# Performance work log

Measured on AMD Instinct MI355X. Metric: run time of the kernel, lower is better.

## Reference

```python
import jax, jax.numpy as jnp
import numpy as np

H = 2048      # hidden_size
F = 768       # moe_intermediate_size
E = 32        # num_experts
K = 4         # num_experts_per_tok (top_k)
SF = 5632     # shared_expert_intermediate_size
B, S = 1, 2048


def setup_inputs() -> dict:
    key = jax.random.key(0)
    ks = jax.random.split(key, 9)
    rn = lambda k, sh, sc: (jax.random.normal(k, sh, jnp.float32) * sc)
    return {
        "hidden_states": rn(ks[0], (B, S, H), 1.0),
        "gate_w": rn(ks[1], (H, E), 0.02),                 # router Linear(H->E), no bias
        "wg": rn(ks[2], (E, H, F), H ** -0.5),             # expert gate_proj
        "wu": rn(ks[3], (E, H, F), H ** -0.5),             # expert up_proj
        "wd": rn(ks[4], (E, F, H), F ** -0.5),             # expert down_proj
        "sg": rn(ks[5], (H, SF), H ** -0.5),               # shared expert gate_proj
        "su": rn(ks[6], (H, SF), H ** -0.5),               # shared expert up_proj
        "sd": rn(ks[7], (SF, H), SF ** -0.5),              # shared expert down_proj
        "seg": rn(ks[8], (H, 1), H ** -0.5),               # shared_expert_gate Linear(H->1)
    }


def _moe_forward(x, gate_w, wg, wu, wd, sg, su, sd, seg):
    # x: [T, H] flattened tokens
    T = x.shape[0]
    logits = x @ gate_w                                    # [T, E]
    probs = jax.nn.softmax(logits, axis=-1)
    topw, topi = jax.lax.top_k(probs, K)                   # [T, K]
    topw = topw / jnp.sum(topw, axis=-1, keepdims=True)    # norm_topk_prob=True
    # dense combine weights [T, E] (expert ids per token are unique -> set is safe)
    combine = jnp.zeros((T, E), x.dtype).at[jnp.arange(T)[:, None], topi].set(topw)

    def body(acc, ew):
        wg_e, wu_e, wd_e, c_e = ew                         # [H,F],[H,F],[F,H],[T]
        h = jax.nn.silu(x @ wg_e) * (x @ wu_e)             # [T, F]
        return acc + c_e[:, None] * (h @ wd_e), None

    out, _ = jax.lax.scan(body, jnp.zeros_like(x), (wg, wu, wd, combine.T))

    shared = (jax.nn.silu(x @ sg) * (x @ su)) @ sd         # [T, H]
    out = out + jax.nn.sigmoid(x @ seg) * shared
    return out


def reference(hidden_states, gate_w, wg, wu, wd, sg, su, sd, seg):
    b, s, h = hidden_states.shape
    x = hidden_states.reshape(-1, h)
    out = _moe_forward(x, gate_w, wg, wu, wd, sg, su, sd, seg)
    return out.reshape(b, s, h)
```

## Files before the change

kernel.cpp:

```cpp
#include <hip/hip_runtime.h>
#include <hip/hip_bf16.h>
#include <math.h>

#define H_DIM 2048
#define F_DIM 768
#define E_NUM 32
#define TOPK 4
#define SF_DIM 5632
#define T_NUM 2048
#define P_MAX (T_NUM * TOPK)
#define KSPLIT 4

#define NB_GU_SHARED ((SF_DIM / 64) * (T_NUM / 128))
#define NB_GU_EXPERT ((F_DIM / 64) * (T_NUM / 128) * E_NUM)
#define NB_DN_SHARED ((H_DIM / 128) * (T_NUM / 128) * KSPLIT)
#define NB_DN_EXPERT ((H_DIM / 128) * (T_NUM / 128) * E_NUM)

typedef __attribute__((ext_vector_type(8))) short short8v;
typedef __attribute__((ext_vector_type(4))) float f4;
typedef unsigned short u16;

__device__ __forceinline__ u16 f2b(float f) {
  unsigned int u = __float_as_uint(f);
  u += 0x7FFFu + ((u >> 16) & 1u);
  return (u16)(u >> 16);
}

__device__ __forceinline__ f4 mfma16(short8v a, short8v b, f4 c) {
  return __builtin_amdgcn_mfma_f32_16x16x32_bf16(a, b, c, 0, 0, 0);
}

__device__ __forceinline__ void gld16(const u16* g, u16* l) {
  __builtin_amdgcn_global_load_lds(
      (const __attribute__((address_space(1))) void*)g,
      (__attribute__((address_space(3))) void*)l, 16, 0, 0);
}

__global__ __launch_bounds__(64) void router_kernel(
    const float* __restrict__ x, const float* __restrict__ gate_w,
    const float* __restrict__ seg, int* __restrict__ cnt,
    int* __restrict__ toklist, int* __restrict__ slotE,
    int* __restrict__ slotPos, float* __restrict__ wt4,
    float* __restrict__ sigbuf) {
  const int t = blockIdx.x;
  const int l = threadIdx.x;
  const int e = l & 31;
  const int half = l >> 5;
  const float* xr = x + (size_t)t * H_DIM;

  float acc = 0.0f, aseg = 0.0f;
  const int h0 = half * (H_DIM / 2);
  for (int h = 0; h < H_DIM / 2; ++h) {
    float xv = xr[h0 + h];
    acc += xv * gate_w[(h0 + h) * E_NUM + e];
    aseg += xv * seg[h0 + h];
  }
  acc += __shfl_xor(acc, 32, 64);
  aseg += __shfl_xor(aseg, 32, 64);

  float m = acc;
#pragma unroll
  for (int mask = 16; mask >= 1; mask >>= 1) m = fmaxf(m, __shfl_xor(m, mask, 64));
  float p = expf(acc - m);
  float s = p;
#pragma unroll
  for (int mask = 16; mask >= 1; mask >>= 1) s += __shfl_xor(s, mask, 64);
  p /= s;

  float pv = p;
  int ids[TOPK];
  float wv[TOPK];
  float wsum = 0.0f;
#pragma unroll
  for (int k = 0; k < TOPK; ++k) {
    float mv = pv;
    int mi = e;
#pragma unroll
    for (int mask = 16; mask >= 1; mask >>= 1) {
      float ov = __shfl_xor(mv, mask, 64);
      int oi = __shfl_xor(mi, mask, 64);
      if (ov > mv || (ov == mv && oi < mi)) { mv = ov; mi = oi; }
    }
    ids[k] = mi;
    wv[k] = mv;
    wsum += mv;
    if (e == mi) pv = -1.0f;
  }

  if (l < TOPK) {
    int id = ids[l];
    float w = wv[l] / wsum;
    int pos = atomicAdd(&cnt[id], 1);
    toklist[id * T_NUM + pos] = t;
    slotE[t * TOPK + l] = id;
    slotPos[t * TOPK + l] = pos;
    wt4[t * TOPK + l] = w;
  }
  if (l == 0) sigbuf[t] = 1.0f / (1.0f + expf(-aseg));
}

__global__ void offs_kernel(const int* __restrict__ cnt, int* __restrict__ offs) {
  if (threadIdx.x == 0) {
    int s = 0;
    for (int e = 0; e < E_NUM; ++e) { offs[e] = s; s += cnt[e]; }
  }
}

__global__ __launch_bounds__(256) void cvt_x(const float* __restrict__ in,
                                             u16* __restrict__ out) {
  int i = blockIdx.x * 256 + threadIdx.x;
  const float4* p = (const float4*)in + (size_t)i * 2;
  float4 a = p[0], b = p[1];
  short8v o;
  o[0] = (short)f2b(a.x); o[1] = (short)f2b(a.y);
  o[2] = (short)f2b(a.z); o[3] = (short)f2b(a.w);
  o[4] = (short)f2b(b.x); o[5] = (short)f2b(b.y);
  o[6] = (short)f2b(b.z); o[7] = (short)f2b(b.w);
  *(short8v*)(out + (size_t)i * 8) = o;
}

__global__ __launch_bounds__(256) void transpose_cvt(
    const float* __restrict__ in, u16* __restrict__ out, int R, int C) {
  in += (size_t)blockIdx.z * R * C;
  out += (size_t)blockIdx.z * R * C;
  const int r0 = blockIdx.y * 64;
  const int c0 = blockIdx.x * 64;
  __shared__ u16 tile[64][72];
  const int tid = threadIdx.x;
  const int tr = tid >> 2, tseg = tid & 3;
  const float* ip = in + (size_t)(r0 + tr) * C + c0 + tseg * 16;
#pragma unroll
  for (int j = 0; j < 4; ++j) {
    float4 v = *(const float4*)(ip + j * 4);
    u16* d = &tile[tr][tseg * 16 + j * 4];
    d[0] = f2b(v.x); d[1] = f2b(v.y); d[2] = f2b(v.z); d[3] = f2b(v.w);
  }
  __syncthreads();
  u16 tmp[16];
#pragma unroll
  for (int j = 0; j < 16; ++j) tmp[j] = tile[tseg * 16 + j][tr];
  u16* op = out + (size_t)(c0 + tr) * R + r0 + tseg * 16;
  *(short8v*)op = *(short8v*)&tmp[0];
  *(short8v*)(op + 8) = *(short8v*)&tmp[8];
}

__global__ __launch_bounds__(256) void gemm_gu_all(
    const u16* __restrict__ A, const u16* __restrict__ sgT,
    const u16* __restrict__ suT, u16* __restrict__ HsOut,
    const u16* __restrict__ wgT, const u16* __restrict__ wuT,
    u16* __restrict__ HeOut, const int* __restrict__ cnt,
    const int* __restrict__ toklist, const int* __restrict__ offs) {
  const int bid = blockIdx.x;
  const int K = H_DIM;
  const u16 *Bg, *Bu;
  u16* Hout;
  int n0, mtile, count, obase, N, gather, e = 0;
  if (bid < NB_GU_SHARED) {
    mtile = bid / (SF_DIM / 64);
    n0 = (bid % (SF_DIM / 64)) * 64;
    count = 1 << 30; obase = 0; N = SF_DIM; gather = 0;
    Bg = sgT; Bu = suT; Hout = HsOut;
  } else {
    const int r = bid - NB_GU_SHARED;
    e = r / ((F_DIM / 64) * (T_NUM / 128));
    const int rem = r % ((F_DIM / 64) * (T_NUM / 128));
    mtile = rem / (F_DIM / 64);
    n0 = (rem % (F_DIM / 64)) * 64;
    count = cnt[e];
    if (mtile * 128 >= count) return;
    obase = offs[e]; N = F_DIM; gather = 1;
    Bg = wgT + (size_t)e * F_DIM * H_DIM;
    Bu = wuT + (size_t)e * F_DIM * H_DIM;
    Hout = HeOut;
  }

  __shared__ u16 As[128 * 32];
  __shared__ u16 Bgs[64 * 32];
  __shared__ u16 Bus[64 * 32];
  __shared__ int ids[128];

  const int tid = threadIdx.x;
  if (tid < 128) {
    int idx = mtile * 128 + tid;
    ids[tid] = gather ? toklist[e * T_NUM + min(idx, count - 1)] : idx;
  }
  __syncthreads();

  const int s = tid & 3, r0 = tid >> 2;
  const int cA0 = (s + (r0 >> 1)) & 3;
  const int cA1 = (s + ((r0 + 64) >> 1)) & 3;
  const u16* ap0 = A + (size_t)ids[r0] * K + cA0 * 8;
  const u16* ap1 = A + (size_t)ids[r0 + 64] * K + cA1 * 8;
  u16* al0 = As + tid * 8;
  u16* al1 = As + tid * 8 + 2048;
  const u16* bgp = Bg + (size_t)(n0 + r0) * K + cA0 * 8;
  const u16* bup = Bu + (size_t)(n0 + r0) * K + cA0 * 8;
  u16* bgl = Bgs + tid * 8;
  u16* bul = Bus + tid * 8;

  const int lane = tid & 63, w = tid >> 6;
  const int w0 = w & 1, w1 = w >> 1;
  const int ln = lane & 15, q = lane >> 4;

  int aoff[4], boff[2];
#pragma unroll
  for (int mt = 0; mt < 4; ++mt) {
    int r = w0 * 64 + mt * 16 + ln;
    aoff[mt] = r * 32 + ((q - (r >> 1)) & 3) * 8;
  }
#pragma unroll
  for (int nt = 0; nt < 2; ++nt) {
    int r = w1 * 32 + nt * 16 + ln;
    boff[nt] = r * 32 + ((q - (r >> 1)) & 3) * 8;
  }

  const f4 zero = {0.f, 0.f, 0.f, 0.f};
  f4 accg[4][2], accu[4][2];
#pragma unroll
  for (int mt = 0; mt < 4; ++mt)
#pragma unroll
    for (int nt = 0; nt < 2; ++nt) { accg[mt][nt] = zero; accu[mt][nt] = zero; }

  for (int k0 = 0; k0 < K; k0 += 32) {
    gld16(ap0 + k0, al0);
    gld16(ap1 + k0, al1);
    gld16(bgp + k0, bgl);
    gld16(bup + k0, bul);
    __syncthreads();
    short8v av[4], bgv[2], buv[2];
#pragma unroll
    for (int mt = 0; mt < 4; ++mt) av[mt] = *(const short8v*)&As[aoff[mt]];
#pragma unroll
    for (int nt = 0; nt < 2; ++nt) {
      bgv[nt] = *(const short8v*)&Bgs[boff[nt]];
      buv[nt] = *(const short8v*)&Bus[boff[nt]];
    }
#pragma unroll
    for (int mt = 0; mt < 4; ++mt)
#pragma unroll
      for (int nt = 0; nt < 2; ++nt) {
        accg[mt][nt] = mfma16(av[mt], bgv[nt], accg[mt][nt]);
        accu[mt][nt] = mfma16(av[mt], buv[nt], accu[mt][nt]);
      }
    __syncthreads();
  }

#pragma unroll
  for (int mt = 0; mt < 4; ++mt)
#pragma unroll
    for (int nt = 0; nt < 2; ++nt)
#pragma unroll
      for (int r = 0; r < 4; ++r) {
        int m = w0 * 64 + mt * 16 + 4 * q + r;
        int idx = mtile * 128 + m;
        if (idx < count) {
          int n = n0 + w1 * 32 + nt * 16 + ln;
          float g = accg[mt][nt][r], u = accu[mt][nt][r];
          float h = g / (1.0f + __expf(-g)) * u;
          Hout[(size_t)(obase + idx) * N + n] = f2b(h);
        }
      }
}

__global__ __launch_bounds__(256) void gemm_dn_all(
    const u16* __restrict__ HsIn, const u16* __restrict__ sdT,
    float* __restrict__ sharedD, const u16* __restrict__ HeIn,
    const u16* __restrict__ wdT, float* __restrict__ Dh,
    const int* __restrict__ cnt, const int* __restrict__ offs) {
  const int bid = blockIdx.x;
  const u16 *Ap, *Bt;
  float* D;
  int n0, mtile, count, obase, K, kbeg, klen, gather;
  if (bid < NB_DN_SHARED) {
    const int kz = bid / ((H_DIM / 128) * (T_NUM / 128));
    const int rem = bid % ((H_DIM / 128) * (T_NUM / 128));
    mtile = rem / (H_DIM / 128);
    n0 = (rem % (H_DIM / 128)) * 128;
    count = 1 << 30; obase = 0; gather = 0;
    K = SF_DIM; klen = SF_DIM / KSPLIT; kbeg = kz * klen;
    Ap = HsIn; Bt = sdT;
    D = sharedD + (size_t)kz * T_NUM * H_DIM;
  } else {
    const int r = bid - NB_DN_SHARED;
    const int e = r / ((H_DIM / 128) * (T_NUM / 128));
    const int rem = r % ((H_DIM / 128) * (T_NUM / 128));
    mtile = rem / (H_DIM / 128);
    n0 = (rem % (H_DIM / 128)) * 128;
    count = cnt[e];
    if (mtile * 128 >= count) return;
    obase = offs[e]; gather = 1;
    K = F_DIM; klen = F_DIM; kbeg = 0;
    Ap = HeIn; Bt = wdT + (size_t)e * H_DIM * F_DIM;
    D = Dh;
  }

  __shared__ u16 As[128 * 32];
  __shared__ u16 Bs[128 * 32];
  __shared__ int ids[128];

  const int tid = threadIdx.x;
  if (tid < 128) {
    int idx = mtile * 128 + tid;
    ids[tid] = gather ? (obase + min(idx, count - 1)) : idx;
  }
  __syncthreads();

  const int s = tid & 3, r0 = tid >> 2;
  const int cA0 = (s + (r0 >> 1)) & 3;
  const int cA1 = (s + ((r0 + 64) >> 1)) & 3;
  const u16* ap0 = Ap + (size_t)ids[r0] * K + kbeg + cA0 * 8;
  const u16* ap1 = Ap + (size_t)ids[r0 + 64] * K + kbeg + cA1 * 8;
  u16* al0 = As + tid * 8;
  u16* al1 = As + tid * 8 + 2048;
  const u16* bp0 = Bt + (size_t)(n0 + r0) * K + kbeg + cA0 * 8;
  const u16* bp1 = Bt + (size_t)(n0 + r0 + 64) * K + kbeg + cA1 * 8;
  u16* bl0 = Bs + tid * 8;
  u16* bl1 = Bs + tid * 8 + 2048;

  const int lane = tid & 63, w = tid >> 6;
  const int w0 = w & 1, w1 = w >> 1;
  const int ln = lane & 15, q = lane >> 4;

  int aoff[4], boff[4];
#pragma unroll
  for (int mt = 0; mt < 4; ++mt) {
    int r = w0 * 64 + mt * 16 + ln;
    aoff[mt] = r * 32 + ((q - (r >> 1)) & 3) * 8;
    int rb = w1 * 64 + mt * 16 + ln;
    boff[mt] = rb * 32 + ((q - (rb >> 1)) & 3) * 8;
  }

  const f4 zero = {0.f, 0.f, 0.f, 0.f};
  f4 acc[4][4];
#pragma unroll
  for (int mt = 0; mt < 4; ++mt)
#pragma unroll
    for (int nt = 0; nt < 4; ++nt) acc[mt][nt] = zero;

  for (int k0 = 0; k0 < klen; k0 += 32) {
    gld16(ap0 + k0, al0);
    gld16(ap1 + k0, al1);
    gld16(bp0 + k0, bl0);
    gld16(bp1 + k0, bl1);
    __syncthreads();
    short8v av[4], bv[4];
#pragma unroll
    for (int i = 0; i < 4; ++i) {
      av[i] = *(const short8v*)&As[aoff[i]];
      bv[i] = *(const short8v*)&Bs[boff[i]];
    }
#pragma unroll
    for (int mt = 0; mt < 4; ++mt)
#pragma unroll
      for (int nt = 0; nt < 4; ++nt)
        acc[mt][nt] = mfma16(av[mt], bv[nt], acc[mt][nt]);
    __syncthreads();
  }

#pragma unroll
  for (int mt = 0; mt < 4; ++mt)
#pragma unroll
    for (int nt = 0; nt < 4; ++nt)
#pragma unroll
      for (int r = 0; r < 4; ++r) {
        int m = w0 * 64 + mt * 16 + 4 * q + r;
        int idx = mtile * 128 + m;
        if (idx < count) {
          int n = n0 + w1 * 64 + nt * 16 + ln;
          D[(size_t)(obase + idx) * H_DIM + n] = acc[mt][nt][r];
        }
      }
}

__global__ __launch_bounds__(256) void combine_kernel(
    const float* __restrict__ sD, const float* __restrict__ Dh,
    const float* __restrict__ sig, const float* __restrict__ wt4,
    const int* __restrict__ slotE, const int* __restrict__ slotPos,
    const int* __restrict__ offs, float* __restrict__ out) {
  const int t = blockIdx.x;
  const int c = threadIdx.x * 8;
  const float sg = sig[t];
  float o[8] = {0.f, 0.f, 0.f, 0.f, 0.f, 0.f, 0.f, 0.f};
#pragma unroll
  for (int z = 0; z < KSPLIT; ++z) {
    const float* sp = sD + ((size_t)z * T_NUM + t) * H_DIM + c;
    float4 a0 = *(const float4*)sp;
    float4 a1 = *(const float4*)(sp + 4);
    o[0] += a0.x; o[1] += a0.y; o[2] += a0.z; o[3] += a0.w;
    o[4] += a1.x; o[5] += a1.y; o[6] += a1.z; o[7] += a1.w;
  }
#pragma unroll
  for (int j = 0; j < 8; ++j) o[j] *= sg;
#pragma unroll
  for (int k = 0; k < TOPK; ++k) {
    int ee = slotE[t * TOPK + k];
    int pp = offs[ee] + slotPos[t * TOPK + k];
    float w = wt4[t * TOPK + k];
    const float* dp = Dh + (size_t)pp * H_DIM + c;
    float4 d0 = *(const float4*)dp;
    float4 d1 = *(const float4*)(dp + 4);
    o[0] += w * d0.x; o[1] += w * d0.y; o[2] += w * d0.z; o[3] += w * d0.w;
    o[4] += w * d1.x; o[5] += w * d1.y; o[6] += w * d1.z; o[7] += w * d1.w;
  }
  float* op = out + (size_t)t * H_DIM + c;
  float4 r0 = {o[0], o[1], o[2], o[3]};
  float4 r1 = {o[4], o[5], o[6], o[7]};
  *(float4*)op = r0;
  *(float4*)(op + 4) = r1;
}

extern "C" void kernel_launch(void* const* d_in, const int* in_sizes, int n_in,
                              void* d_out, int out_size, void* d_ws, size_t ws_size,
                              hipStream_t stream) {
  const float* x      = (const float*)d_in[0];
  const float* gate_w = (const float*)d_in[1];
  const float* wg     = (const float*)d_in[2];
  const float* wu     = (const float*)d_in[3];
  const float* wd     = (const float*)d_in[4];
  const float* sg     = (const float*)d_in[5];
  const float* su     = (const float*)d_in[6];
  const float* sd     = (const float*)d_in[7];
  const float* seg    = (const float*)d_in[8];
  float* out = (float*)d_out;

  char* p = (char*)d_ws;
  auto alloc = [&](size_t bytes) {
    char* r = p;
    p += (bytes + 255) & ~(size_t)255;
    return r;
  };
  int* cnt      = (int*)alloc(E_NUM * 4);
  int* offs     = (int*)alloc(E_NUM * 4);
  int* toklist  = (int*)alloc((size_t)E_NUM * T_NUM * 4);
  int* slotE    = (int*)alloc((size_t)T_NUM * TOPK * 4);
  int* slotPos  = (int*)alloc((size_t)T_NUM * TOPK * 4);
  float* wt4    = (float*)alloc((size_t)T_NUM * TOPK * 4);
  float* sigbuf = (float*)alloc((size_t)T_NUM * 4);
  u16* xb  = (u16*)alloc((size_t)T_NUM * H_DIM * 2);
  u16* sgT = (u16*)alloc((size_t)H_DIM * SF_DIM * 2);
  u16* suT = (u16*)alloc((size_t)H_DIM * SF_DIM * 2);
  u16* sdT = (u16*)alloc((size_t)H_DIM * SF_DIM * 2);
  u16* wgT = (u16*)alloc((size_t)E_NUM * H_DIM * F_DIM * 2);
  u16* wuT = (u16*)alloc((size_t)E_NUM * H_DIM * F_DIM * 2);
  u16* wdT = (u16*)alloc((size_t)E_NUM * H_DIM * F_DIM * 2);
  u16* Hs  = (u16*)alloc((size_t)T_NUM * SF_DIM * 2);
  u16* He  = (u16*)alloc((size_t)(P_MAX + 128) * F_DIM * 2);
  float* sharedD = (float*)alloc((size_t)KSPLIT * T_NUM * H_DIM * 4);
  float* Dh      = (float*)alloc((size_t)P_MAX * H_DIM * 4);

  hipMemsetAsync(cnt, 0, E_NUM * 4, stream);
  router_kernel<<<T_NUM, 64, 0, stream>>>(x, gate_w, seg, cnt, toklist,
                                          slotE, slotPos, wt4, sigbuf);
  offs_kernel<<<1, 64, 0, stream>>>(cnt, offs);

  cvt_x<<<(T_NUM * H_DIM / 8) / 256, 256, 0, stream>>>(x, xb);
  transpose_cvt<<<dim3(SF_DIM / 64, H_DIM / 64, 1), 256, 0, stream>>>(sg, sgT, H_DIM, SF_DIM);
  transpose_cvt<<<dim3(SF_DIM / 64, H_DIM / 64, 1), 256, 0, stream>>>(su, suT, H_DIM, SF_DIM);
  transpose_cvt<<<dim3(H_DIM / 64, SF_DIM / 64, 1), 256, 0, stream>>>(sd, sdT, SF_DIM, H_DIM);
  transpose_cvt<<<dim3(F_DIM / 64, H_DIM / 64, E_NUM), 256, 0, stream>>>(wg, wgT, H_DIM, F_DIM);
  transpose_cvt<<<dim3(F_DIM / 64, H_DIM / 64, E_NUM), 256, 0, stream>>>(wu, wuT, H_DIM, F_DIM);
  transpose_cvt<<<dim3(H_DIM / 64, F_DIM / 64, E_NUM), 256, 0, stream>>>(wd, wdT, F_DIM, H_DIM);

  gemm_gu_all<<<NB_GU_SHARED + NB_GU_EXPERT, 256, 0, stream>>>(
      xb, sgT, suT, Hs, wgT, wuT, He, cnt, toklist, offs);
  gemm_dn_all<<<NB_DN_SHARED + NB_DN_EXPERT, 256, 0, stream>>>(
      Hs, sdT, sharedD, He, wdT, Dh, cnt, offs);

  combine_kernel<<<T_NUM, 256, 0, stream>>>(sharedD, Dh, sigbuf, wt4,
                                            slotE, slotPos, offs, out);
}
```

Baseline: 1.199 ms.

## Double-buffer LDS tiles in gate-up and down MoE GEMMs

Both grouped GEMM kernels now use two LDS buffers and issue the direct global-to-LDS loads for the next K-slice before running the MFMAs on the current one. This overlaps memory latency with compute and halves the number of barriers per K-step. It doubles LDS use per block, which may lower occupancy, and it assumes the K lengths are multiples of 64.

```diff
diff --git a/kernel.cpp b/kernel.cpp
--- a/kernel.cpp
+++ b/kernel.cpp
@@ -143,6 +143,33 @@
   *(short8v*)op = *(short8v*)&tmp[0];
   *(short8v*)(op + 8) = *(short8v*)&tmp[8];
 }
+
+#define STAGE_GU(Ab, Bgb, Bub, kk)        \
+  {                                       \
+    gld16(ap0 + (kk), Ab + tid * 8);      \
+    gld16(ap1 + (kk), Ab + tid * 8 + 2048); \
+    gld16(bgp + (kk), Bgb + tid * 8);     \
+    gld16(bup + (kk), Bub + tid * 8);     \
+  }
+
+#define COMP_GU(Ab, Bgb, Bub)                                              \
+  {                                                                        \
+    short8v av[4], bgv[2], buv[2];                                         \
+    _Pragma("unroll")                                                      \
+    for (int mt = 0; mt < 4; ++mt) av[mt] = *(const short8v*)&Ab[aoff[mt]]; \
+    _Pragma("unroll")                                                      \
+    for (int nt = 0; nt < 2; ++nt) {                                       \
+      bgv[nt] = *(const short8v*)&Bgb[boff[nt]];                           \
+      buv[nt] = *(const short8v*)&Bub[boff[nt]];                           \
+    }                                                                      \
+    _Pragma("unroll")                                                      \
+    for (int mt = 0; mt < 4; ++mt)                                         \
+      _Pragma("unroll")                                                    \
+      for (int nt = 0; nt < 2; ++nt) {                                     \
+        accg[mt][nt] = mfma16(av[mt], bgv[nt], accg[mt][nt]);              \
+        accu[mt][nt] = mfma16(av[mt], buv[nt], accu[mt][nt]);              \
+      }                                                                    \
+  }
 
 __global__ __launch_bounds__(256) void gemm_gu_all(
     const u16* __restrict__ A, const u16* __restrict__ sgT,
@@ -174,9 +201,9 @@
     Hout = HeOut;
   }
 
-  __shared__ u16 As[128 * 32];
-  __shared__ u16 Bgs[64 * 32];
-  __shared__ u16 Bus[64 * 32];
+  __shared__ u16 As0[128 * 32], As1[128 * 32];
+  __shared__ u16 Bgs0[64 * 32], Bgs1[64 * 32];
+  __shared__ u16 Bus0[64 * 32], Bus1[64 * 32];
   __shared__ int ids[128];
 
   const int tid = threadIdx.x;
@@ -191,12 +218,8 @@
   const int cA1 = (s + ((r0 + 64) >> 1)) & 3;
   const u16* ap0 = A + (size_t)ids[r0] * K + cA0 * 8;
   const u16* ap1 = A + (size_t)ids[r0 + 64] * K + cA1 * 8;
-  u16* al0 = As + tid * 8;
-  u16* al1 = As + tid * 8 + 2048;
   const u16* bgp = Bg + (size_t)(n0 + r0) * K + cA0 * 8;
   const u16* bup = Bu + (size_t)(n0 + r0) * K + cA0 * 8;
-  u16* bgl = Bgs + tid * 8;
-  u16* bul = Bus + tid * 8;
 
   const int lane = tid & 63, w = tid >> 6;
   const int w0 = w & 1, w1 = w >> 1;
@@ -221,27 +244,14 @@
 #pragma unroll
     for (int nt = 0; nt < 2; ++nt) { accg[mt][nt] = zero; accu[mt][nt] = zero; }
 
-  for (int k0 = 0; k0 < K; k0 += 32) {
-    gld16(ap0 + k0, al0);
-    gld16(ap1 + k0, al1);
-    gld16(bgp + k0, bgl);
-    gld16(bup + k0, bul);
+  STAGE_GU(As0, Bgs0, Bus0, 0);
+  __syncthreads();
+  for (int k0 = 0; k0 < K; k0 += 64) {
+    STAGE_GU(As1, Bgs1, Bus1, k0 + 32);
+    COMP_GU(As0, Bgs0, Bus0);
     __syncthreads();
-    short8v av[4], bgv[2], buv[2];
-#pragma unroll
-    for (int mt = 0; mt < 4; ++mt) av[mt] = *(const short8v*)&As[aoff[mt]];
-#pragma unroll
-    for (int nt = 0; nt < 2; ++nt) {
-      bgv[nt] = *(const short8v*)&Bgs[boff[nt]];
-      buv[nt] = *(const short8v*)&Bus[boff[nt]];
-    }
-#pragma unroll
-    for (int mt = 0; mt < 4; ++mt)
-#pragma unroll
-      for (int nt = 0; nt < 2; ++nt) {
-        accg[mt][nt] = mfma16(av[mt], bgv[nt], accg[mt][nt]);
-        accu[mt][nt] = mfma16(av[mt], buv[nt], accu[mt][nt]);
-      }
+    if (k0 + 64 < K) STAGE_GU(As0, Bgs0, Bus0, k0 + 64);
+    COMP_GU(As1, Bgs1, Bus1);
     __syncthreads();
   }
 
@@ -261,6 +271,29 @@
         }
       }
 }
+
+#define STAGE_DN(Ab, Bb, kk)               \
+  {                                        \
+    gld16(ap0 + (kk), Ab + tid * 8);       \
+    gld16(ap1 + (kk), Ab + tid * 8 + 2048);\
+    gld16(bp0 + (kk), Bb + tid * 8);       \
+    gld16(bp1 + (kk), Bb + tid * 8 + 2048);\
+  }
+
+#define COMP_DN(Ab, Bb)                                                     \
+  {                                                                         \
+    short8v av[4], bv[4];                                                   \
+    _Pragma("unroll")                                                       \
+    for (int i = 0; i < 4; ++i) {                                           \
+      av[i] = *(const short8v*)&Ab[aoff[i]];                                \
+      bv[i] = *(const short8v*)&Bb[boff[i]];                                \
+    }                                                                       \
+    _Pragma("unroll")                                                       \
+    for (int mt = 0; mt < 4; ++mt)                                          \
+      _Pragma("unroll")                                                     \
+      for (int nt = 0; nt < 4; ++nt)                                        \
+        acc[mt][nt] = mfma16(av[mt], bv[nt], acc[mt][nt]);                  \
+  }
 
 __global__ __launch_bounds__(256) void gemm_dn_all(
     const u16* __restrict__ HsIn, const u16* __restrict__ sdT,
@@ -294,8 +327,8 @@
     D = Dh;
   }
 
-  __shared__ u16 As[128 * 32];
-  __shared__ u16 Bs[128 * 32];
+  __shared__ u16 As0[128 * 32], As1[128 * 32];
+  __shared__ u16 Bs0[128 * 32], Bs1[128 * 32];
   __shared__ int ids[128];
 
   const int tid = threadIdx.x;
@@ -310,12 +343,8 @@
   const int cA1 = (s + ((r0 + 64) >> 1)) & 3;
   const u16* ap0 = Ap + (size_t)ids[r0] * K + kbeg + cA0 * 8;
   const u16* ap1 = Ap + (size_t)ids[r0 + 64] * K + kbeg + cA1 * 8;
-  u16* al0 = As + tid * 8;
-  u16* al1 = As + tid * 8 + 2048;
   const u16* bp0 = Bt + (size_t)(n0 + r0) * K + kbeg + cA0 * 8;
   const u16* bp1 = Bt + (size_t)(n0 + r0 + 64) * K + kbeg + cA1 * 8;
-  u16* bl0 = Bs + tid * 8;
-  u16* bl1 = Bs + tid * 8 + 2048;
 
   const int lane = tid & 63, w = tid >> 6;
   const int w0 = w & 1, w1 = w >> 1;
@@ -337,23 +366,14 @@
 #pragma unroll
     for (int nt = 0; nt < 4; ++nt) acc[mt][nt] = zero;
 
-  for (int k0 = 0; k0 < klen; k0 += 32) {
-    gld16(ap0 + k0, al0);
-    gld16(ap1 + k0, al1);
-    gld16(bp0 + k0, bl0);
-    gld16(bp1 + k0, bl1);
+  STAGE_DN(As0, Bs0, 0);
+  __syncthreads();
+  for (int k0 = 0; k0 < klen; k0 += 64) {
+    STAGE_DN(As1, Bs1, k0 + 32);
+    COMP_DN(As0, Bs0);
     __syncthreads();
-    short8v av[4], bv[4];
-#pragma unroll
-    for (int i = 0; i < 4; ++i) {
-      av[i] = *(const short8v*)&As[aoff[i]];
-      bv[i] = *(const short8v*)&Bs[boff[i]];
-    }
-#pragma unroll
-    for (int mt = 0; mt < 4; ++mt)
-#pragma unroll
-      for (int nt = 0; nt < 4; ++nt)
-        acc[mt][nt] = mfma16(av[mt], bv[nt], acc[mt][nt]);
+    if (k0 + 64 < klen) STAGE_DN(As0, Bs0, k0 + 64);
+    COMP_DN(As1, Bs1);
     __syncthreads();
   }
 
```

New measurement: 1.236 ms. +3.1%, slower.

## Fuse combine into down-projection epilogue via scaled atomic adds to output

Applied to the files above, without the earlier changes.

Removes the separate combine kernel and the intermediate fp32 buffers for the shared split-K partials and per-slot expert outputs. The down-projection epilogue now scales each row by its routing weight or the shared sigmoid gate and atomically adds it into the zeroed output. The router stores weights per expert slot instead of per token. This cuts large fp32 writes and reads, but adds many float atomics with contention across split-K and expert contributions, and the summation order is no longer deterministic.

```diff
diff --git a/kernel.cpp b/kernel.cpp
--- a/kernel.cpp
+++ b/kernel.cpp
@@ -39,8 +39,7 @@
 __global__ __launch_bounds__(64) void router_kernel(
     const float* __restrict__ x, const float* __restrict__ gate_w,
     const float* __restrict__ seg, int* __restrict__ cnt,
-    int* __restrict__ toklist, int* __restrict__ slotE,
-    int* __restrict__ slotPos, float* __restrict__ wt4,
+    int* __restrict__ toklist, float* __restrict__ wtslot,
     float* __restrict__ sigbuf) {
   const int t = blockIdx.x;
   const int l = threadIdx.x;
@@ -92,9 +91,7 @@
     float w = wv[l] / wsum;
     int pos = atomicAdd(&cnt[id], 1);
     toklist[id * T_NUM + pos] = t;
-    slotE[t * TOPK + l] = id;
-    slotPos[t * TOPK + l] = pos;
-    wt4[t * TOPK + l] = w;
+    wtslot[id * T_NUM + pos] = w;
   }
   if (l == 0) sigbuf[t] = 1.0f / (1.0f + expf(-aseg));
 }
@@ -264,13 +261,13 @@
 
 __global__ __launch_bounds__(256) void gemm_dn_all(
     const u16* __restrict__ HsIn, const u16* __restrict__ sdT,
-    float* __restrict__ sharedD, const u16* __restrict__ HeIn,
-    const u16* __restrict__ wdT, float* __restrict__ Dh,
-    const int* __restrict__ cnt, const int* __restrict__ offs) {
+    const u16* __restrict__ HeIn, const u16* __restrict__ wdT,
+    const int* __restrict__ cnt, const int* __restrict__ offs,
+    const int* __restrict__ toklist, const float* __restrict__ wtslot,
+    const float* __restrict__ sigbuf, float* __restrict__ out) {
   const int bid = blockIdx.x;
   const u16 *Ap, *Bt;
-  float* D;
-  int n0, mtile, count, obase, K, kbeg, klen, gather;
+  int n0, mtile, count, obase, K, kbeg, klen, gather, e = 0;
   if (bid < NB_DN_SHARED) {
     const int kz = bid / ((H_DIM / 128) * (T_NUM / 128));
     const int rem = bid % ((H_DIM / 128) * (T_NUM / 128));
@@ -279,10 +276,9 @@
     count = 1 << 30; obase = 0; gather = 0;
     K = SF_DIM; klen = SF_DIM / KSPLIT; kbeg = kz * klen;
     Ap = HsIn; Bt = sdT;
-    D = sharedD + (size_t)kz * T_NUM * H_DIM;
   } else {
     const int r = bid - NB_DN_SHARED;
-    const int e = r / ((H_DIM / 128) * (T_NUM / 128));
+    e = r / ((H_DIM / 128) * (T_NUM / 128));
     const int rem = r % ((H_DIM / 128) * (T_NUM / 128));
     mtile = rem / (H_DIM / 128);
     n0 = (rem % (H_DIM / 128)) * 128;
@@ -291,7 +287,6 @@
     obase = offs[e]; gather = 1;
     K = F_DIM; klen = F_DIM; kbeg = 0;
     Ap = HeIn; Bt = wdT + (size_t)e * H_DIM * F_DIM;
-    D = Dh;
   }
 
   __shared__ u16 As[128 * 32];
@@ -360,53 +355,27 @@
 #pragma unroll
   for (int mt = 0; mt < 4; ++mt)
 #pragma unroll
-    for (int nt = 0; nt < 4; ++nt)
-#pragma unroll
-      for (int r = 0; r < 4; ++r) {
-        int m = w0 * 64 + mt * 16 + 4 * q + r;
-        int idx = mtile * 128 + m;
-        if (idx < count) {
+    for (int r = 0; r < 4; ++r) {
+      int m = w0 * 64 + mt * 16 + 4 * q + r;
+      int idx = mtile * 128 + m;
+      if (idx < count) {
+        int t;
+        float scale;
+        if (gather) {
+          t = toklist[e * T_NUM + idx];
+          scale = wtslot[e * T_NUM + idx];
+        } else {
+          t = idx;
+          scale = sigbuf[idx];
+        }
+        float* orow = out + (size_t)t * H_DIM;
+#pragma unroll
+        for (int nt = 0; nt < 4; ++nt) {
           int n = n0 + w1 * 64 + nt * 16 + ln;
-          D[(size_t)(obase + idx) * H_DIM + n] = acc[mt][nt][r];
+          atomicAdd(&orow[n], acc[mt][nt][r] * scale);
         }
       }
-}
-
-__global__ __launch_bounds__(256) void combine_kernel(
-    const float* __restrict__ sD, const float* __restrict__ Dh,
-    const float* __restrict__ sig, const float* __restrict__ wt4,
-    const int* __restrict__ slotE, const int* __restrict__ slotPos,
-    const int* __restrict__ offs, float* __restrict__ out) {
-  const int t = blockIdx.x;
-  const int c = threadIdx.x * 8;
-  const float sg = sig[t];
-  float o[8] = {0.f, 0.f, 0.f, 0.f, 0.f, 0.f, 0.f, 0.f};
-#pragma unroll
-  for (int z = 0; z < KSPLIT; ++z) {
-    const float* sp = sD + ((size_t)z * T_NUM + t) * H_DIM + c;
-    float4 a0 = *(const float4*)sp;
-    float4 a1 = *(const float4*)(sp + 4);
-    o[0] += a0.x; o[1] += a0.y; o[2] += a0.z; o[3] += a0.w;
-    o[4] += a1.x; o[5] += a1.y; o[6] += a1.z; o[7] += a1.w;
-  }
-#pragma unroll
-  for (int j = 0; j < 8; ++j) o[j] *= sg;
-#pragma unroll
-  for (int k = 0; k < TOPK; ++k) {
-    int ee = slotE[t * TOPK + k];
-    int pp = offs[ee] + slotPos[t * TOPK + k];
-    float w = wt4[t * TOPK + k];
-    const float* dp = Dh + (size_t)pp * H_DIM + c;
-    float4 d0 = *(const float4*)dp;
-    float4 d1 = *(const float4*)(dp + 4);
-    o[0] += w * d0.x; o[1] += w * d0.y; o[2] += w * d0.z; o[3] += w * d0.w;
-    o[4] += w * d1.x; o[5] += w * d1.y; o[6] += w * d1.z; o[7] += w * d1.w;
-  }
-  float* op = out + (size_t)t * H_DIM + c;
-  float4 r0 = {o[0], o[1], o[2], o[3]};
-  float4 r1 = {o[4], o[5], o[6], o[7]};
-  *(float4*)op = r0;
-  *(float4*)(op + 4) = r1;
+    }
 }
 
 extern "C" void kernel_launch(void* const* d_in, const int* in_sizes, int n_in,
@@ -432,9 +401,7 @@
   int* cnt      = (int*)alloc(E_NUM * 4);
   int* offs     = (int*)alloc(E_NUM * 4);
   int* toklist  = (int*)alloc((size_t)E_NUM * T_NUM * 4);
-  int* slotE    = (int*)alloc((size_t)T_NUM * TOPK * 4);
-  int* slotPos  = (int*)alloc((size_t)T_NUM * TOPK * 4);
-  float* wt4    = (float*)alloc((size_t)T_NUM * TOPK * 4);
+  float* wtslot = (float*)alloc((size_t)E_NUM * T_NUM * 4);
   float* sigbuf = (float*)alloc((size_t)T_NUM * 4);
   u16* xb  = (u16*)alloc((size_t)T_NUM * H_DIM * 2);
   u16* sgT = (u16*)alloc((size_t)H_DIM * SF_DIM * 2);
@@ -445,12 +412,11 @@
   u16* wdT = (u16*)alloc((size_t)E_NUM * H_DIM * F_DIM * 2);
   u16* Hs  = (u16*)alloc((size_t)T_NUM * SF_DIM * 2);
   u16* He  = (u16*)alloc((size_t)(P_MAX + 128) * F_DIM * 2);
-  float* sharedD = (float*)alloc((size_t)KSPLIT * T_NUM * H_DIM * 4);
-  float* Dh      = (float*)alloc((size_t)P_MAX * H_DIM * 4);
 
   hipMemsetAsync(cnt, 0, E_NUM * 4, stream);
+  hipMemsetAsync(out, 0, (size_t)T_NUM * H_DIM * 4, stream);
   router_kernel<<<T_NUM, 64, 0, stream>>>(x, gate_w, seg, cnt, toklist,
-                                          slotE, slotPos, wt4, sigbuf);
+                                          wtslot, sigbuf);
   offs_kernel<<<1, 64, 0, stream>>>(cnt, offs);
 
   cvt_x<<<(T_NUM * H_DIM / 8) / 256, 256, 0, stream>>>(x, xb);
@@ -464,8 +430,5 @@
   gemm_gu_all<<<NB_GU_SHARED + NB_GU_EXPERT, 256, 0, stream>>>(
       xb, sgT, suT, Hs, wgT, wuT, He, cnt, toklist, offs);
   gemm_dn_all<<<NB_DN_SHARED + NB_DN_EXPERT, 256, 0, stream>>>(
-      Hs, sdT, sharedD, He, wdT, Dh, cnt, offs);
-
-  combine_kernel<<<T_NUM, 256, 0, stream>>>(sharedD, Dh, sigbuf, wt4,
-                                            slotE, slotPos, offs, out);
-}
+      Hs, sdT, He, wdT, cnt, offs, toklist, wtslot, sigbuf, out);
+}
```

Measured after the change: 1.239 ms. 1.03x slower.
